# Kernel tuning notes

Measured on AMD Instinct MI355X. Metric: run time of the kernel, lower is better.

## Reference

```python
import jax, jax.numpy as jnp
import numpy as np

N, H, E, A, T = 50000, 128, 800000, 16, 4


def setup_inputs() -> dict:
    key = jax.random.key(0)
    ks = jax.random.split(key, 12)
    s = 1.0 / np.sqrt(H + A)
    s2 = 1.0 / np.sqrt(H)
    return {
        "h": jax.random.normal(ks[0], (N, H), dtype=jnp.float32),
        "edge_index": jax.random.randint(ks[1], (2, E), 0, N, dtype=jnp.int32),
        "edge_type": jax.random.randint(ks[2], (E,), 0, T, dtype=jnp.int32),
        "edge_attr": jax.random.normal(ks[3], (E, A), dtype=jnp.float32),
        # per-edge-type 2-layer MLP params
        "W1": jax.random.uniform(ks[4], (T, H + A, H), minval=-s, maxval=s, dtype=jnp.float32),
        "b1": jax.random.uniform(ks[5], (T, H), minval=-s, maxval=s, dtype=jnp.float32),
        "W2": jax.random.uniform(ks[6], (T, H, H), minval=-s2, maxval=s2, dtype=jnp.float32),
        "b2": jax.random.uniform(ks[7], (T, H), minval=-s2, maxval=s2, dtype=jnp.float32),
        # GRUCell params (torch layout: [3H, H] with gate order r, z, n)
        "w_ih": jax.random.uniform(ks[8], (3 * H, H), minval=-s2, maxval=s2, dtype=jnp.float32),
        "w_hh": jax.random.uniform(ks[9], (3 * H, H), minval=-s2, maxval=s2, dtype=jnp.float32),
        "b_ih": jax.random.uniform(ks[10], (3 * H,), minval=-s2, maxval=s2, dtype=jnp.float32),
        "b_hh": jax.random.uniform(ks[11], (3 * H,), minval=-s2, maxval=s2, dtype=jnp.float32),
    }


def reference(h, edge_index, edge_type, edge_attr, W1, b1, W2, b2, w_ih, w_hh, b_ih, b_hh):
    src, dst = edge_index[0], edge_index[1]
    h_in = jnp.concatenate([h[src], edge_attr], axis=-1)  # [E, H+A]
    # per-edge-type MLP; loop over small fixed num_edge_types, mask-select
    m = jnp.zeros((h_in.shape[0], H), dtype=h.dtype)
    for t in range(T):
        mt = jax.nn.relu(h_in @ W1[t] + b1[t]) @ W2[t] + b2[t]  # [E, H]
        m = jnp.where((edge_type == t)[:, None], mt, m)
    # scatter-add messages to destination nodes
    msg = jax.ops.segment_sum(m, dst, num_segments=h.shape[0])  # [N, H]
    # GRUCell(msg, h) with torch gate order r, z, n
    gi = msg @ w_ih.T + b_ih  # [N, 3H]
    gh = h @ w_hh.T + b_hh
    i_r, i_z, i_n = jnp.split(gi, 3, axis=-1)
    h_r, h_z, h_n = jnp.split(gh, 3, axis=-1)
    r = jax.nn.sigmoid(i_r + h_r)
    z = jax.nn.sigmoid(i_z + h_z)
    n = jnp.tanh(i_n + r * h_n)
    return (1.0 - z) * n + z * h
```

## Files before the change

### kernel.cpp

```cpp
#include <hip/hip_runtime.h>
#include <stdint.h>

#define Hh 128
#define Aa 16
#define Tt 4
#define K1 144
#define K1P 160
#define W1T_LD 168
#define WG_LD  136

typedef float f32x4 __attribute__((ext_vector_type(4)));
typedef __bf16 bf16x8 __attribute__((ext_vector_type(8)));
typedef unsigned short u16x8 __attribute__((ext_vector_type(8)));
typedef unsigned short u16x4 __attribute__((ext_vector_type(4)));

static __device__ __forceinline__ unsigned short f2bf(float f) {
    unsigned u = __builtin_bit_cast(unsigned, f);
    u += 0x7fffu + ((u >> 16) & 1u);
    return (unsigned short)(u >> 16);
}

static __device__ __forceinline__ float bf2f(unsigned short u) {
    return __builtin_bit_cast(float, (unsigned)u << 16);
}

static __device__ __forceinline__ bf16x8 pack8(const float* __restrict__ x) {
    f32x4 a = *(const f32x4*)x;
    f32x4 b = *(const f32x4*)(x + 4);
    u16x8 t;
    t[0] = f2bf(a[0]); t[1] = f2bf(a[1]); t[2] = f2bf(a[2]); t[3] = f2bf(a[3]);
    t[4] = f2bf(b[0]); t[5] = f2bf(b[1]); t[6] = f2bf(b[2]); t[7] = f2bf(b[3]);
    return __builtin_bit_cast(bf16x8, t);
}

static __device__ __forceinline__ bf16x8 zero_bf8() {
    u16x8 z = {0, 0, 0, 0, 0, 0, 0, 0};
    return __builtin_bit_cast(bf16x8, z);
}

__global__ void cast_all_kernel(
    const float* __restrict__ h, const float* __restrict__ wih, const float* __restrict__ whh,
    unsigned short* __restrict__ h_bf, unsigned short* __restrict__ wihb,
    unsigned short* __restrict__ whhb, int n0, int n1, int n2)
{
    int i = blockIdx.x * blockDim.x + threadIdx.x;
    if (i >= n2) return;
    const float* s; unsigned short* d; int off;
    if (i < n0)      { s = h;   d = h_bf; off = i; }
    else if (i < n1) { s = wih; d = wihb; off = i - n0; }
    else             { s = whh; d = whhb; off = i - n1; }
    f32x4 v = *(const f32x4*)(s + (size_t)off * 4);
    u16x4 o;
    o[0] = f2bf(v[0]); o[1] = f2bf(v[1]); o[2] = f2bf(v[2]); o[3] = f2bf(v[3]);
    *(u16x4*)(d + (size_t)off * 4) = o;
}

__global__ void w1t_kernel(const float* __restrict__ W1, unsigned short* __restrict__ W1Tbf) {
    __shared__ float tile[16][129];
    const int b = blockIdx.x;
    const int t = b / 10, kb = b % 10;
    const int k0 = kb * 16;
    const int tid = threadIdx.x;
    for (int e = tid; e < 16 * 128; e += 256) {
        int k = e >> 7, n = e & 127;
        tile[k][n] = (k0 + k < K1) ? W1[((size_t)t * K1 + k0 + k) * Hh + n] : 0.f;
    }
    __syncthreads();
    for (int e = tid; e < 128 * 16; e += 256) {
        int n = e >> 4, kk = e & 15;
        W1Tbf[((size_t)t * Hh + n) * K1P + k0 + kk] = f2bf(tile[kk][n]);
    }
}

__global__ void w2t_kernel(const float* __restrict__ W2, unsigned short* __restrict__ W2Tbf) {
    __shared__ float tile[16][129];
    const int b = blockIdx.x;
    const int t = b >> 3, kb = b & 7;
    const int k0 = kb * 16;
    const int tid = threadIdx.x;
    for (int e = tid; e < 16 * 128; e += 256) {
        int k = e >> 7, n = e & 127;
        tile[k][n] = W2[((size_t)t * Hh + k0 + k) * Hh + n];
    }
    __syncthreads();
    for (int e = tid; e < 128 * 16; e += 256) {
        int n = e >> 4, kk = e & 15;
        W2Tbf[((size_t)t * Hh + n) * Hh + k0 + kk] = f2bf(tile[kk][n]);
    }
}

__global__ void hist_kernel(const int* __restrict__ et, const int* __restrict__ eidx,
                            int E, int N, int* __restrict__ cnt, unsigned* __restrict__ rank) {
    for (int i = blockIdx.x * blockDim.x + threadIdx.x; i < E; i += gridDim.x * blockDim.x) {
        rank[i] = (unsigned)atomicAdd(&cnt[et[i] * N + eidx[E + i]], 1);
    }
}

__global__ void scanA_kernel(const int* __restrict__ deg2, int nb, int* __restrict__ bsum) {
    __shared__ int red[256];
    const int t = threadIdx.x;
    const int i0 = blockIdx.x * 1024 + t * 4;
    int s = 0;
    #pragma unroll
    for (int j = 0; j < 4; j++) if (i0 + j < nb) s += deg2[i0 + j];
    red[t] = s; __syncthreads();
    for (int d = 128; d > 0; d >>= 1) {
        if (t < d) red[t] += red[t + d];
        __syncthreads();
    }
    if (t == 0) bsum[blockIdx.x] = red[0];
}

__global__ void scanB_kernel(int* __restrict__ bsum, int nblocks,
                             int* __restrict__ rowptrD, int fourN, int E) {
    __shared__ int ts[512];
    const int t = threadIdx.x;
    int v = (t < nblocks) ? bsum[t] : 0;
    ts[t] = v; __syncthreads();
    for (int d = 1; d < 512; d <<= 1) {
        int x = (t >= d) ? ts[t - d] : 0;
        __syncthreads();
        ts[t] += x;
        __syncthreads();
    }
    if (t < nblocks) bsum[t] = ts[t] - v;
    if (t == 0) rowptrD[fourN] = E;
}

__global__ void scanC_kernel(int* __restrict__ cur, int nb,
                             const int* __restrict__ bsum, int* __restrict__ rowptrD) {
    __shared__ int ts[256];
    const int t = threadIdx.x;
    const int i0 = blockIdx.x * 1024 + t * 4;
    int v[4];
    #pragma unroll
    for (int j = 0; j < 4; j++) v[j] = (i0 + j < nb) ? cur[i0 + j] : 0;
    int s = v[0] + v[1] + v[2] + v[3];
    ts[t] = s; __syncthreads();
    for (int d = 1; d < 256; d <<= 1) {
        int x = (t >= d) ? ts[t - d] : 0;
        __syncthreads();
        ts[t] += x;
        __syncthreads();
    }
    int run = bsum[blockIdx.x] + ts[t] - s;
    #pragma unroll
    for (int j = 0; j < 4; j++) {
        if (i0 + j < nb) {
            rowptrD[i0 + j] = run;
            cur[i0 + j] = run;
            run += v[j];
        }
    }
}

__global__ void fill2_kernel(const int* __restrict__ et, const int* __restrict__ eidx,
                             int E, int N, const int* __restrict__ binstart,
                             const unsigned* __restrict__ rank, int2* __restrict__ rec) {
    for (int i = blockIdx.x * blockDim.x + threadIdx.x; i < E; i += gridDim.x * blockDim.x) {
        int posD = binstart[et[i] * N + eidx[E + i]] + (int)rank[i];
        rec[posD] = make_int2(eidx[i], i);
    }
}

__global__ __launch_bounds__(512) void l1_kernel(
    const unsigned short* __restrict__ h_bf, const int2* __restrict__ rec,
    const float* __restrict__ eattr, const unsigned short* __restrict__ W1Tbf,
    const float* __restrict__ b1, const int* __restrict__ rowptrD,
    unsigned short* __restrict__ Yg, int N)
{
    __shared__ unsigned short W1T[128 * W1T_LD];
    __shared__ float b1s[128];
    const int t = blockIdx.x & 3;
    const int lb = blockIdx.x >> 2;
    const int nbk = gridDim.x >> 2;
    const int tid = threadIdx.x;

    for (int idx = tid; idx < (Hh * K1P) / 8; idx += 512) {
        int n = idx / 20, c = (idx % 20) * 8;
        *(u16x8*)&W1T[n * W1T_LD + c] =
            *(const u16x8*)&W1Tbf[((size_t)t * Hh + n) * K1P + c];
    }
    if (tid < 128) b1s[tid] = b1[t * Hh + tid];
    __syncthreads();

    const int tstart = rowptrD[t * N];
    const int tend = rowptrD[(t + 1) * N];
    const int cnt = tend - tstart;
    const int ntiles = (cnt + 255) >> 8;
    const int w = tid >> 6, lane = tid & 63;
    const int l15 = lane & 15, q = lane >> 4;
    const int tl = tend - 1;

    for (int tile = lb; tile < ntiles; tile += nbk) {
        __builtin_amdgcn_sched_barrier(0);
        const int p0 = tstart + tile * 256 + w * 32;
        const int pa = p0 + l15, pb = p0 + 16 + l15;
        const bool va = pa < tend, vb = pb < tend;
        const int2 ra = rec[min(pa, tl)];
        const int2 rb = rec[min(pb, tl)];
        const unsigned short* __restrict__ hA = h_bf + (size_t)ra.x * Hh;
        const unsigned short* __restrict__ hB = h_bf + (size_t)rb.x * Hh;

        f32x4 acc[8][2];
        #pragma unroll
        for (int mt = 0; mt < 8; mt++) {
            acc[mt][0] = (f32x4){0.f, 0.f, 0.f, 0.f};
            acc[mt][1] = (f32x4){0.f, 0.f, 0.f, 0.f};
        }

        #pragma unroll
        for (int ks = 0; ks < 5; ks++) {
            const int k0 = ks * 32;
            bf16x8 fb_a, fb_b;
            if (ks < 4) {
                fb_a = __builtin_bit_cast(bf16x8, *(const u16x8*)(hA + k0 + q * 8));
                fb_b = __builtin_bit_cast(bf16x8, *(const u16x8*)(hB + k0 + q * 8));
            } else if (q < 2) {
                fb_a = pack8(eattr + (size_t)ra.y * Aa + q * 8);
                fb_b = pack8(eattr + (size_t)rb.y * Aa + q * 8);
            } else {
                fb_a = zero_bf8();
                fb_b = zero_bf8();
            }
            #pragma unroll
            for (int mt = 0; mt < 8; mt++) {
                bf16x8 fa = *(const bf16x8*)&W1T[(mt * 16 + l15) * W1T_LD + k0 + q * 8];
                acc[mt][0] = __builtin_amdgcn_mfma_f32_16x16x32_bf16(fa, fb_a, acc[mt][0], 0, 0, 0);
                acc[mt][1] = __builtin_amdgcn_mfma_f32_16x16x32_bf16(fa, fb_b, acc[mt][1], 0, 0, 0);
            }
        }
        __builtin_amdgcn_sched_barrier(0);

        #pragma unroll
        for (int g = 0; g < 2; g++) {
            if (g ? vb : va) {
                unsigned short* __restrict__ o = Yg + (size_t)(g ? pb : pa) * Hh + q * 4;
                #pragma unroll
                for (int mt = 0; mt < 8; mt++) {
                    f32x4 bias = *(const f32x4*)&b1s[mt * 16 + q * 4];
                    u16x4 y;
                    #pragma unroll
                    for (int i = 0; i < 4; i++) {
                        float v = acc[mt][g][i] + bias[i];
                        y[i] = f2bf(v > 0.f ? v : 0.f);
                    }
                    *(u16x4*)(o + mt * 16) = y;
                }
            }
        }
        __builtin_amdgcn_sched_barrier(0);
    }
}

__global__ __launch_bounds__(256) void zgemm_kernel(
    const unsigned short* __restrict__ Yg, const int* __restrict__ rowptrD,
    const unsigned short* __restrict__ W2Tbf, const float* __restrict__ b2,
    unsigned short* __restrict__ msgb, int N)
{
    __shared__ unsigned short W2T[128 * WG_LD];
    __shared__ float b2s[512];
    __shared__ int cntS[4 * 64];
    const int tid = threadIdx.x;
    const int w = tid >> 6, lane = tid & 63;
    const int l15 = lane & 15, q = lane >> 4;
    const int nodebase = blockIdx.x * 64 + w * 16;
    const int nA = min(nodebase + l15, N - 1);

    b2s[tid] = b2[tid];
    b2s[tid + 256] = b2[tid + 256];

    f32x4 acc[8];
    #pragma unroll
    for (int ct = 0; ct < 8; ct++) acc[ct] = (f32x4){0.f, 0.f, 0.f, 0.f};

    for (int t = 0; t < Tt; t++) {
        __syncthreads();
        for (int idx = tid; idx < (Hh * Hh) / 8; idx += 256) {
            int n = idx >> 4, c = (idx & 15) * 8;
            *(u16x8*)&W2T[n * WG_LD + c] =
                *(const u16x8*)&W2Tbf[((size_t)t * Hh + n) * Hh + c];
        }
        __syncthreads();

        const int seg = rowptrD[(size_t)t * N + nA];
        const int len = rowptrD[(size_t)t * N + nA + 1] - seg;
        cntS[w * 64 + t * 16 + l15] = len;

        float asum[32];
        #pragma unroll
        for (int i = 0; i < 32; i++) asum[i] = 0.f;
        for (int j = 0; j < len; j++) {
            const unsigned short* __restrict__ yr = Yg + (size_t)(seg + j) * Hh;
            #pragma unroll
            for (int ks = 0; ks < 4; ks++) {
                u16x8 yv = *(const u16x8*)(yr + ks * 32 + q * 8);
                #pragma unroll
                for (int e = 0; e < 8; e++) asum[ks * 8 + e] += bf2f(yv[e]);
            }
        }

        #pragma unroll
        for (int ks = 0; ks < 4; ks++) {
            u16x8 fr;
            #pragma unroll
            for (int e = 0; e < 8; e++) fr[e] = f2bf(asum[ks * 8 + e]);
            bf16x8 fa = __builtin_bit_cast(bf16x8, fr);
            #pragma unroll
            for (int ct = 0; ct < 8; ct++) {
                bf16x8 fb = *(const bf16x8*)&W2T[(ct * 16 + l15) * WG_LD + ks * 32 + q * 8];
                acc[ct] = __builtin_amdgcn_mfma_f32_16x16x32_bf16(fa, fb, acc[ct], 0, 0, 0);
            }
        }
    }
    __syncthreads();

    #pragma unroll
    for (int ct = 0; ct < 8; ct++) {
        const int c = ct * 16 + l15;
        #pragma unroll
        for (int i = 0; i < 4; i++) {
            int node = nodebase + q * 4 + i;
            if (node < N) {
                float bias = 0.f;
                #pragma unroll
                for (int t = 0; t < Tt; t++)
                    bias += (float)cntS[w * 64 + t * 16 + q * 4 + i] * b2s[t * 128 + c];
                msgb[(size_t)node * Hh + c] = f2bf(acc[ct][i] + bias);
            }
        }
    }
}

__global__ __launch_bounds__(512) void gru_kernel(
    const float* __restrict__ h, const unsigned short* __restrict__ h_bf,
    const unsigned short* __restrict__ msgb,
    const unsigned short* __restrict__ wihb, const unsigned short* __restrict__ whhb,
    const float* __restrict__ b_ih, const float* __restrict__ b_hh,
    float* __restrict__ out, int N)
{
    __shared__ unsigned short Wg[128 * WG_LD];
    const int tid = threadIdx.x;
    const int lane = tid & 63;
    const int l15 = lane & 15, q = lane >> 4;
    const int w = tid >> 6;
    const int nodebase = blockIdx.x * 128 + w * 16;
    const int nA = min(nodebase + l15, N - 1);

    bf16x8 fm[4], fh[4];
    #pragma unroll
    for (int ks = 0; ks < 4; ks++) {
        fm[ks] = __builtin_bit_cast(bf16x8, *(const u16x8*)(msgb + (size_t)nA * Hh + ks * 32 + q * 8));
        fh[ks] = __builtin_bit_cast(bf16x8, *(const u16x8*)(h_bf + (size_t)nA * Hh + ks * 32 + q * 8));
    }

    u16x8 pre[4];
    const int so = tid >> 4, sk = (tid & 15) * 8;
    auto loadg = [&](const unsigned short* __restrict__ Ws, int gate) {
        #pragma unroll
        for (int i = 0; i < 4; i++)
            pre[i] = *(const u16x8*)&Ws[(size_t)gate * Hh * Hh + (size_t)(so + i * 32) * Hh + sk];
    };
    auto commit = [&]() {
        __syncthreads();
        #pragma unroll
        for (int i = 0; i < 4; i++)
            *(u16x8*)&Wg[(so + i * 32) * WG_LD + sk] = pre[i];
        __syncthreads();
    };
    auto matmul = [&](f32x4* acc, const bf16x8* fa) {
        #pragma unroll
        for (int ks = 0; ks < 4; ks++) {
            #pragma unroll
            for (int ct = 0; ct < 8; ct++) {
                bf16x8 fb = *(const bf16x8*)&Wg[(ct * 16 + l15) * WG_LD + ks * 32 + q * 8];
                acc[ct] = __builtin_amdgcn_mfma_f32_16x16x32_bf16(fa[ks], fb, acc[ct], 0, 0, 0);
            }
        }
    };

    f32x4 gr[8], gin[8], ghn[8];
    #pragma unroll
    for (int ct = 0; ct < 8; ct++) {
        gr[ct] = (f32x4){0.f, 0.f, 0.f, 0.f};
        gin[ct] = (f32x4){0.f, 0.f, 0.f, 0.f};
        ghn[ct] = (f32x4){0.f, 0.f, 0.f, 0.f};
    }

    loadg(wihb, 0);
    commit(); loadg(whhb, 0); matmul(gr, fm);
    commit(); loadg(wihb, 2); matmul(gr, fh);
    commit(); loadg(whhb, 2); matmul(gin, fm);
    commit(); loadg(wihb, 1); matmul(ghn, fh);

    #pragma unroll
    for (int ct = 0; ct < 8; ct++) {
        const int c = ct * 16 + l15;
        float bir = b_ih[c], bhr = b_hh[c];
        float bin = b_ih[256 + c], bhn = b_hh[256 + c];
        #pragma unroll
        for (int i = 0; i < 4; i++) {
            float rv = 1.f / (1.f + __expf(-(gr[ct][i] + bir + bhr)));
            gin[ct][i] = gin[ct][i] + bin + rv * (ghn[ct][i] + bhn);
        }
    }
    #pragma unroll
    for (int ct = 0; ct < 8; ct++) gr[ct] = (f32x4){0.f, 0.f, 0.f, 0.f};

    commit(); loadg(whhb, 1); matmul(gr, fm);
    commit();                 matmul(gr, fh);

    #pragma unroll
    for (int ct = 0; ct < 8; ct++) {
        const int c = ct * 16 + l15;
        float biz = b_ih[128 + c], bhz = b_hh[128 + c];
        #pragma unroll
        for (int i = 0; i < 4; i++) {
            int node = nodebase + q * 4 + i;
            if (node < N) {
                float zv = 1.f / (1.f + __expf(-(gr[ct][i] + biz + bhz)));
                float e2 = __expf(-2.f * gin[ct][i]);
                float nv = (1.f - e2) / (1.f + e2);
                float hv = h[(size_t)node * Hh + c];
                out[(size_t)node * Hh + c] = (1.f - zv) * nv + zv * hv;
            }
        }
    }
}

static inline size_t align256(size_t x) { return (x + 255) & ~(size_t)255; }

extern "C" void kernel_launch(void* const* d_in, const int* in_sizes, int n_in,
                              void* d_out, int out_size, void* d_ws, size_t ws_size,
                              hipStream_t stream)
{
    const float* h     = (const float*)d_in[0];
    const int*   eidx  = (const int*)d_in[1];
    const int*   et    = (const int*)d_in[2];
    const float* eattr = (const float*)d_in[3];
    const float* W1    = (const float*)d_in[4];
    const float* b1    = (const float*)d_in[5];
    const float* W2    = (const float*)d_in[6];
    const float* b2    = (const float*)d_in[7];
    const float* w_ih  = (const float*)d_in[8];
    const float* w_hh  = (const float*)d_in[9];
    const float* b_ih  = (const float*)d_in[10];
    const float* b_hh  = (const float*)d_in[11];

    const int N = in_sizes[0] / Hh;
    const int E = in_sizes[1] / 2;
    const int nb = 4 * N;
    const int sblocks = (nb + 1023) / 1024;

    char* p = (char*)d_ws;
    unsigned short* msgb = (unsigned short*)p; p += align256((size_t)N * Hh * sizeof(unsigned short));
    unsigned short* Yg = (unsigned short*)p;   p += align256((size_t)E * Hh * sizeof(unsigned short));
    int2* rec = (int2*)p;               p += align256((size_t)E * sizeof(int2));
    unsigned* rank = (unsigned*)p;      p += align256((size_t)E * sizeof(unsigned));
    int* rowptrD = (int*)p;             p += align256(((size_t)4 * N + 1) * sizeof(int));
    int* cur = (int*)p;                 p += align256((size_t)nb * sizeof(int));
    int* bsum = (int*)p;                p += align256(1024 * sizeof(int));
    unsigned short* h_bf = (unsigned short*)p; p += align256((size_t)N * Hh * sizeof(unsigned short));
    unsigned short* W1Tbf = (unsigned short*)p; p += align256((size_t)Tt * Hh * K1P * sizeof(unsigned short));
    unsigned short* W2Tbf = (unsigned short*)p; p += align256((size_t)Tt * Hh * Hh * sizeof(unsigned short));
    unsigned short* wihb = (unsigned short*)p; p += align256((size_t)3 * Hh * Hh * sizeof(unsigned short));
    unsigned short* whhb = (unsigned short*)p; p += align256((size_t)3 * Hh * Hh * sizeof(unsigned short));

    hipMemsetAsync(cur, 0, (size_t)nb * sizeof(int), stream);

    {
        int n4h = N * Hh / 4, n4g = 3 * Hh * Hh / 4;
        int c0 = n4h, c1 = c0 + n4g, c2 = c1 + n4g;
        cast_all_kernel<<<(c2 + 255) / 256, 256, 0, stream>>>(
            h, w_ih, w_hh, h_bf, wihb, whhb, c0, c1, c2);
    }
    w1t_kernel<<<Tt * 10, 256, 0, stream>>>(W1, W1Tbf);
    w2t_kernel<<<Tt * 8, 256, 0, stream>>>(W2, W2Tbf);

    hist_kernel<<<1024, 256, 0, stream>>>(et, eidx, E, N, cur, rank);
    scanA_kernel<<<sblocks, 256, 0, stream>>>(cur, nb, bsum);
    scanB_kernel<<<1, 512, 0, stream>>>(bsum, sblocks, rowptrD, 4 * N, E);
    scanC_kernel<<<sblocks, 256, 0, stream>>>(cur, nb, bsum, rowptrD);
    fill2_kernel<<<1024, 256, 0, stream>>>(et, eidx, E, N, cur, rank, rec);

    l1_kernel<<<2048, 512, 0, stream>>>(h_bf, rec, eattr, W1Tbf, b1, rowptrD, Yg, N);
    zgemm_kernel<<<(N + 63) / 64, 256, 0, stream>>>(Yg, rowptrD, W2Tbf, b2, msgb, N);

    int gblocks = (N + 127) / 128;
    gru_kernel<<<gblocks, 512, 0, stream>>>(h, h_bf, msgb, wihb, whhb, b_ih, b_hh, (float*)d_out, N);
}
```

Baseline: 447.5 us.

## Pre-cast edge attributes to bf16 and launch one l1 block per tile

Edge attributes are now cast to bf16 once in the shared cast kernel, so l1 loads packed bf16 instead of converting fp32 in its inner loop. The l1 kernel drops its persistent grid-stride loop over tiles. It launches about E/256 blocks, and each block finds its edge type and tile by walking the per-type tile counts. This removes per-tile looping and the uneven per-type work split, but every block now reloads the full W1 slice into LDS for a single tile. It also adds an extra pass over edge_attr and a new workspace buffer.

```diff
diff --git a/kernel.cpp b/kernel.cpp
--- a/kernel.cpp
+++ b/kernel.cpp
@@ -24,31 +24,25 @@
     return __builtin_bit_cast(float, (unsigned)u << 16);
 }
 
-static __device__ __forceinline__ bf16x8 pack8(const float* __restrict__ x) {
-    f32x4 a = *(const f32x4*)x;
-    f32x4 b = *(const f32x4*)(x + 4);
-    u16x8 t;
-    t[0] = f2bf(a[0]); t[1] = f2bf(a[1]); t[2] = f2bf(a[2]); t[3] = f2bf(a[3]);
-    t[4] = f2bf(b[0]); t[5] = f2bf(b[1]); t[6] = f2bf(b[2]); t[7] = f2bf(b[3]);
-    return __builtin_bit_cast(bf16x8, t);
-}
-
 static __device__ __forceinline__ bf16x8 zero_bf8() {
     u16x8 z = {0, 0, 0, 0, 0, 0, 0, 0};
     return __builtin_bit_cast(bf16x8, z);
 }
 
 __global__ void cast_all_kernel(
-    const float* __restrict__ h, const float* __restrict__ wih, const float* __restrict__ whh,
-    unsigned short* __restrict__ h_bf, unsigned short* __restrict__ wihb,
-    unsigned short* __restrict__ whhb, int n0, int n1, int n2)
+    const float* __restrict__ h, const float* __restrict__ ea,
+    const float* __restrict__ wih, const float* __restrict__ whh,
+    unsigned short* __restrict__ h_bf, unsigned short* __restrict__ ebf,
+    unsigned short* __restrict__ wihb, unsigned short* __restrict__ whhb,
+    int n0, int n1, int n2, int n3)
 {
     int i = blockIdx.x * blockDim.x + threadIdx.x;
-    if (i >= n2) return;
+    if (i >= n3) return;
     const float* s; unsigned short* d; int off;
     if (i < n0)      { s = h;   d = h_bf; off = i; }
-    else if (i < n1) { s = wih; d = wihb; off = i - n0; }
-    else             { s = whh; d = whhb; off = i - n1; }
+    else if (i < n1) { s = ea;  d = ebf;  off = i - n0; }
+    else if (i < n2) { s = wih; d = wihb; off = i - n1; }
+    else             { s = whh; d = whhb; off = i - n2; }
     f32x4 v = *(const f32x4*)(s + (size_t)off * 4);
     u16x4 o;
     o[0] = f2bf(v[0]); o[1] = f2bf(v[1]); o[2] = f2bf(v[2]); o[3] = f2bf(v[3]);
@@ -165,16 +159,23 @@
 
 __global__ __launch_bounds__(512) void l1_kernel(
     const unsigned short* __restrict__ h_bf, const int2* __restrict__ rec,
-    const float* __restrict__ eattr, const unsigned short* __restrict__ W1Tbf,
+    const unsigned short* __restrict__ ebf, const unsigned short* __restrict__ W1Tbf,
     const float* __restrict__ b1, const int* __restrict__ rowptrD,
     unsigned short* __restrict__ Yg, int N)
 {
     __shared__ unsigned short W1T[128 * W1T_LD];
     __shared__ float b1s[128];
-    const int t = blockIdx.x & 3;
-    const int lb = blockIdx.x >> 2;
-    const int nbk = gridDim.x >> 2;
     const int tid = threadIdx.x;
+
+    int rem = blockIdx.x, t = 0, tstart = 0, tend = 0;
+    for (; t < Tt; t++) {
+        tstart = rowptrD[t * N];
+        tend = rowptrD[(t + 1) * N];
+        int ntt = (tend - tstart + 255) >> 8;
+        if (rem < ntt) break;
+        rem -= ntt;
+    }
+    if (t == Tt) return;
 
     for (int idx = tid; idx < (Hh * K1P) / 8; idx += 512) {
         int n = idx / 20, c = (idx % 20) * 8;
@@ -184,72 +185,63 @@
     if (tid < 128) b1s[tid] = b1[t * Hh + tid];
     __syncthreads();
 
-    const int tstart = rowptrD[t * N];
-    const int tend = rowptrD[(t + 1) * N];
-    const int cnt = tend - tstart;
-    const int ntiles = (cnt + 255) >> 8;
     const int w = tid >> 6, lane = tid & 63;
     const int l15 = lane & 15, q = lane >> 4;
     const int tl = tend - 1;
 
-    for (int tile = lb; tile < ntiles; tile += nbk) {
-        __builtin_amdgcn_sched_barrier(0);
-        const int p0 = tstart + tile * 256 + w * 32;
-        const int pa = p0 + l15, pb = p0 + 16 + l15;
-        const bool va = pa < tend, vb = pb < tend;
-        const int2 ra = rec[min(pa, tl)];
-        const int2 rb = rec[min(pb, tl)];
-        const unsigned short* __restrict__ hA = h_bf + (size_t)ra.x * Hh;
-        const unsigned short* __restrict__ hB = h_bf + (size_t)rb.x * Hh;
-
-        f32x4 acc[8][2];
+    const int p0 = tstart + rem * 256 + w * 32;
+    const int pa = p0 + l15, pb = p0 + 16 + l15;
+    const bool va = pa < tend, vb = pb < tend;
+    const int2 ra = rec[min(pa, tl)];
+    const int2 rb = rec[min(pb, tl)];
+    const unsigned short* __restrict__ hA = h_bf + (size_t)ra.x * Hh;
+    const unsigned short* __restrict__ hB = h_bf + (size_t)rb.x * Hh;
+
+    f32x4 acc[8][2];
+    #pragma unroll
+    for (int mt = 0; mt < 8; mt++) {
+        acc[mt][0] = (f32x4){0.f, 0.f, 0.f, 0.f};
+        acc[mt][1] = (f32x4){0.f, 0.f, 0.f, 0.f};
+    }
+
+    #pragma unroll
+    for (int ks = 0; ks < 5; ks++) {
+        const int k0 = ks * 32;
+        bf16x8 fb_a, fb_b;
+        if (ks < 4) {
+            fb_a = __builtin_bit_cast(bf16x8, *(const u16x8*)(hA + k0 + q * 8));
+            fb_b = __builtin_bit_cast(bf16x8, *(const u16x8*)(hB + k0 + q * 8));
+        } else if (q < 2) {
+            fb_a = __builtin_bit_cast(bf16x8, *(const u16x8*)(ebf + (size_t)ra.y * Aa + q * 8));
+            fb_b = __builtin_bit_cast(bf16x8, *(const u16x8*)(ebf + (size_t)rb.y * Aa + q * 8));
+        } else {
+            fb_a = zero_bf8();
+            fb_b = zero_bf8();
+        }
         #pragma unroll
         for (int mt = 0; mt < 8; mt++) {
-            acc[mt][0] = (f32x4){0.f, 0.f, 0.f, 0.f};
-            acc[mt][1] = (f32x4){0.f, 0.f, 0.f, 0.f};
-        }
-
-        #pragma unroll
-        for (int ks = 0; ks < 5; ks++) {
-            const int k0 = ks * 32;
-            bf16x8 fb_a, fb_b;
-            if (ks < 4) {
-                fb_a = __builtin_bit_cast(bf16x8, *(const u16x8*)(hA + k0 + q * 8));
-                fb_b = __builtin_bit_cast(bf16x8, *(const u16x8*)(hB + k0 + q * 8));
-            } else if (q < 2) {
-                fb_a = pack8(eattr + (size_t)ra.y * Aa + q * 8);
-                fb_b = pack8(eattr + (size_t)rb.y * Aa + q * 8);
-            } else {
-                fb_a = zero_bf8();
-                fb_b = zero_bf8();
-            }
+            bf16x8 fa = *(const bf16x8*)&W1T[(mt * 16 + l15) * W1T_LD + k0 + q * 8];
+            acc[mt][0] = __builtin_amdgcn_mfma_f32_16x16x32_bf16(fa, fb_a, acc[mt][0], 0, 0, 0);
+            acc[mt][1] = __builtin_amdgcn_mfma_f32_16x16x32_bf16(fa, fb_b, acc[mt][1], 0, 0, 0);
+        }
+    }
+
+    #pragma unroll
+    for (int g = 0; g < 2; g++) {
+        if (g ? vb : va) {
+            unsigned short* __restrict__ o = Yg + (size_t)(g ? pb : pa) * Hh + q * 4;
             #pragma unroll
             for (int mt = 0; mt < 8; mt++) {
-                bf16x8 fa = *(const bf16x8*)&W1T[(mt * 16 + l15) * W1T_LD + k0 + q * 8];
-                acc[mt][0] = __builtin_amdgcn_mfma_f32_16x16x32_bf16(fa, fb_a, acc[mt][0], 0, 0, 0);
-                acc[mt][1] = __builtin_amdgcn_mfma_f32_16x16x32_bf16(fa, fb_b, acc[mt][1], 0, 0, 0);
-            }
-        }
-        __builtin_amdgcn_sched_barrier(0);
-
-        #pragma unroll
-        for (int g = 0; g < 2; g++) {
-            if (g ? vb : va) {
-                unsigned short* __restrict__ o = Yg + (size_t)(g ? pb : pa) * Hh + q * 4;
+                f32x4 bias = *(const f32x4*)&b1s[mt * 16 + q * 4];
+                u16x4 y;
                 #pragma unroll
-                for (int mt = 0; mt < 8; mt++) {
-                    f32x4 bias = *(const f32x4*)&b1s[mt * 16 + q * 4];
-                    u16x4 y;
-                    #pragma unroll
-                    for (int i = 0; i < 4; i++) {
-                        float v = acc[mt][g][i] + bias[i];
-                        y[i] = f2bf(v > 0.f ? v : 0.f);
-                    }
-                    *(u16x4*)(o + mt * 16) = y;
+                for (int i = 0; i < 4; i++) {
+                    float v = acc[mt][g][i] + bias[i];
+                    y[i] = f2bf(v > 0.f ? v : 0.f);
                 }
-            }
-        }
-        __builtin_amdgcn_sched_barrier(0);
+                *(u16x4*)(o + mt * 16) = y;
+            }
+        }
     }
 }
 
@@ -461,6 +453,7 @@
     int* cur = (int*)p;                 p += align256((size_t)nb * sizeof(int));
     int* bsum = (int*)p;                p += align256(1024 * sizeof(int));
     unsigned short* h_bf = (unsigned short*)p; p += align256((size_t)N * Hh * sizeof(unsigned short));
+    unsigned short* ebf = (unsigned short*)p;  p += align256((size_t)E * Aa * sizeof(unsigned short));
     unsigned short* W1Tbf = (unsigned short*)p; p += align256((size_t)Tt * Hh * K1P * sizeof(unsigned short));
     unsigned short* W2Tbf = (unsigned short*)p; p += align256((size_t)Tt * Hh * Hh * sizeof(unsigned short));
     unsigned short* wihb = (unsigned short*)p; p += align256((size_t)3 * Hh * Hh * sizeof(unsigned short));
@@ -469,10 +462,10 @@
     hipMemsetAsync(cur, 0, (size_t)nb * sizeof(int), stream);
 
     {
-        int n4h = N * Hh / 4, n4g = 3 * Hh * Hh / 4;
-        int c0 = n4h, c1 = c0 + n4g, c2 = c1 + n4g;
-        cast_all_kernel<<<(c2 + 255) / 256, 256, 0, stream>>>(
-            h, w_ih, w_hh, h_bf, wihb, whhb, c0, c1, c2);
+        int n4h = N * Hh / 4, n4e = E * Aa / 4, n4g = 3 * Hh * Hh / 4;
+        int c0 = n4h, c1 = c0 + n4e, c2 = c1 + n4g, c3 = c2 + n4g;
+        cast_all_kernel<<<(c3 + 255) / 256, 256, 0, stream>>>(
+            h, eattr, w_ih, w_hh, h_bf, ebf, wihb, whhb, c0, c1, c2, c3);
     }
     w1t_kernel<<<Tt * 10, 256, 0, stream>>>(W1, W1Tbf);
     w2t_kernel<<<Tt * 8, 256, 0, stream>>>(W2, W2Tbf);
@@ -483,7 +476,8 @@
     scanC_kernel<<<sblocks, 256, 0, stream>>>(cur, nb, bsum, rowptrD);
     fill2_kernel<<<1024, 256, 0, stream>>>(et, eidx, E, N, cur, rank, rec);
 
-    l1_kernel<<<2048, 512, 0, stream>>>(h_bf, rec, eattr, W1Tbf, b1, rowptrD, Yg, N);
+    int l1grid = E / 256 + Tt + 1;
+    l1_kernel<<<l1grid, 512, 0, stream>>>(h_bf, rec, ebf, W1Tbf, b1, rowptrD, Yg, N);
     zgemm_kernel<<<(N + 63) / 64, 256, 0, stream>>>(Yg, rowptrD, W2Tbf, b2, msgb, N);
 
     int gblocks = (N + 127) / 128;
```

Result: faster. 432.7 us (-3.3%).
